# Kernel tuning notes

Measured on AMD Instinct MI355X. Metric: run time of the kernel, lower is better.

Reference implementation:

```python
import jax, jax.numpy as jnp
import numpy as np

N_VOXELS = 262144  # active output voxels (stride=1 -> same coord set as input)


def setup_inputs() -> dict:
    key = jax.random.key(0)
    k1, k2, k3, k4 = jax.random.split(key, 4)
    N, C_IN, C_OUT, K, M = N_VOXELS, 64, 64, 27, 65536
    x = jax.random.normal(k1, (N, C_IN), dtype=jnp.float32)
    W = jax.random.normal(k2, (K, C_IN, C_OUT), dtype=jnp.float32) * (1.0 / np.sqrt(C_IN * K))
    in_map = jax.random.randint(k3, (K, M), 0, N, dtype=jnp.int32)
    out_map = jax.random.randint(k4, (K, M), 0, N, dtype=jnp.int32)
    return {"x": x, "W": W, "in_map": in_map, "out_map": out_map}


def reference(x, W, in_map, out_map):
    # Sparse (Minkowski-style) convolution: gather -> per-offset GEMM -> scatter-add.
    # x: [N, Cin], W: [K, Cin, Cout], in_map/out_map: [K, M] indices into voxel list.
    N = x.shape[0]
    C_out = W.shape[-1]
    gathered = x[in_map]                              # [K, M, Cin]  (irregular gather)
    msg = jnp.einsum('kmc,kcd->kmd', gathered, W)     # [K, M, Cout] per-offset GEMM
    out = jnp.zeros((N, C_out), dtype=x.dtype)
    out = out.at[out_map.reshape(-1)].add(msg.reshape(-1, C_out))  # scatter-add
    return out
```

## Files before the change

kernel.cpp:

```cpp
#include <hip/hip_runtime.h>


typedef __attribute__((ext_vector_type(8))) short bf16x8;
typedef __attribute__((ext_vector_type(8))) unsigned short u16x8;
typedef __attribute__((ext_vector_type(4))) unsigned short u16x4;
typedef __attribute__((ext_vector_type(4))) float f32x4;
typedef __attribute__((ext_vector_type(2))) float f32x2;

constexpr int KOFF = 27;
constexpr int M = 65536;
constexpr int CIN = 64;
constexpr int COUT = 64;
constexpr int NVOX = 262144;
constexpr int NMSG = KOFF * M;
constexpr int TM_BLOCK = 512;
constexpr int TILES_PER_K = M / TM_BLOCK;
constexpr int SUBTILES = TM_BLOCK / (4 * 16);
constexpr int XCVT_BLOCKS = NVOX * CIN / 8 / 256;

static __device__ __forceinline__ short f2bf(float f) {
  unsigned u = __builtin_bit_cast(unsigned, f);
  unsigned r = (u + 0x7FFFu + ((u >> 16) & 1u)) >> 16;
  return (short)r;
}
static __device__ __forceinline__ float bf2f(unsigned short h) {
  return __builtin_bit_cast(float, (unsigned)h << 16);
}

__global__ __launch_bounds__(256) void xw_kernel(
    const float* __restrict__ x, const float* __restrict__ W,
    unsigned short* __restrict__ xb, unsigned short* __restrict__ Wf,
    int xcvtBlocks) {
  const int b = blockIdx.x;
  if (b < xcvtBlocks) {
    int i = b * 256 + threadIdx.x;
    const float4* p = (const float4*)x + (size_t)i * 2;
    float4 a = p[0], q = p[1];
    u16x8 h;
    h[0] = (unsigned short)f2bf(a.x); h[1] = (unsigned short)f2bf(a.y);
    h[2] = (unsigned short)f2bf(a.z); h[3] = (unsigned short)f2bf(a.w);
    h[4] = (unsigned short)f2bf(q.x); h[5] = (unsigned short)f2bf(q.y);
    h[6] = (unsigned short)f2bf(q.z); h[7] = (unsigned short)f2bf(q.w);
    *(u16x8*)(xb + (size_t)i * 8) = h;
  } else {
    int k = b - xcvtBlocks;
    const float* Wk = W + (size_t)k * (CIN * COUT);
    unsigned short* dst = Wf + (size_t)k * 4096;
#pragma unroll
    for (int i = 0; i < 16; ++i) {
      int e = threadIdx.x * 16 + i;
      int j = e & 7, l = (e >> 3) & 63, tu = e >> 9;
      int t = tu >> 1, u = tu & 1;
      dst[e] = (unsigned short)f2bf(Wk[(u * 32 + (l >> 4) * 8 + j) * COUT + t * 16 + (l & 15)]);
    }
  }
}

__global__ __launch_bounds__(256) void rank_kernel(const int* __restrict__ out_map,
                                                   int* __restrict__ cnt,
                                                   int* __restrict__ rank) {
  int i = (blockIdx.x * 256 + threadIdx.x) * 4;
  int4 om = *(const int4*)(out_map + i);
  int4 rk;
  rk.x = atomicAdd(&cnt[om.x], 1);
  rk.y = atomicAdd(&cnt[om.y], 1);
  rk.z = atomicAdd(&cnt[om.z], 1);
  rk.w = atomicAdd(&cnt[om.w], 1);
  *(int4*)(rank + i) = rk;
}

__global__ __launch_bounds__(256) void scan1_kernel(const int* __restrict__ cnt,
                                                    int* __restrict__ starts,
                                                    int* __restrict__ blockSums) {
  __shared__ int s[256];
  int t = threadIdx.x, i = blockIdx.x * 256 + t;
  int c = cnt[i];
  s[t] = c; __syncthreads();
  for (int off = 1; off < 256; off <<= 1) {
    int add = (t >= off) ? s[t - off] : 0;
    __syncthreads(); s[t] += add; __syncthreads();
  }
  starts[i] = s[t] - c;
  if (t == 255) blockSums[blockIdx.x] = s[t];
}

__global__ __launch_bounds__(256) void scan2_kernel(int* __restrict__ bs) {
  __shared__ int s[256];
  int t = threadIdx.x;
  int v0 = bs[t*4], v1 = bs[t*4+1], v2 = bs[t*4+2], v3 = bs[t*4+3];
  int sum = v0 + v1 + v2 + v3;
  s[t] = sum; __syncthreads();
  for (int off = 1; off < 256; off <<= 1) {
    int add = (t >= off) ? s[t - off] : 0;
    __syncthreads(); s[t] += add; __syncthreads();
  }
  int run = s[t] - sum;
  bs[t*4] = run; run += v0;
  bs[t*4+1] = run; run += v1;
  bs[t*4+2] = run; run += v2;
  bs[t*4+3] = run;
}

__global__ __launch_bounds__(256) void scan3_kernel(int* __restrict__ starts,
                                                    const int* __restrict__ blockBase) {
  int i = blockIdx.x * 256 + threadIdx.x;
  starts[i] += blockBase[blockIdx.x];
  if (i == 0) starts[NVOX] = NMSG;
}

template <bool BF16IN>
__global__ __launch_bounds__(256) void gemm_msg_kernel(
    const void* __restrict__ xin, const unsigned short* __restrict__ Wf,
    const int* __restrict__ in_map, const int* __restrict__ out_map,
    const int* __restrict__ rank, const int* __restrict__ starts,
    unsigned short* __restrict__ msg) {
  const int k = blockIdx.x / TILES_PER_K;
  const int mblock = (blockIdx.x % TILES_PER_K) * TM_BLOCK;
  const int wave = threadIdx.x >> 6;
  const int l = threadIdx.x & 63;
  const int lg = l >> 4;
  const int lr = l & 15;

  bf16x8 bfrag[4][2];
  const bf16x8* wf = (const bf16x8*)(Wf + (size_t)k * 4096);
#pragma unroll
  for (int t = 0; t < 4; ++t)
#pragma unroll
    for (int u = 0; u < 2; ++u)
      bfrag[t][u] = wf[(t * 2 + u) * 64 + l];

  const int mwave = mblock + wave * (TM_BLOCK / 4);
  const int rb = k * M + mwave;

  auto loadA = [&](int s, bf16x8& A0, bf16x8& A1) {
    int id = in_map[rb + s * 16 + lr];
    if (BF16IN) {
      const unsigned short* xr = (const unsigned short*)xin + (size_t)id * CIN + lg * 8;
      A0 = *(const bf16x8*)(xr);
      A1 = *(const bf16x8*)(xr + 32);
    } else {
      const float* xr = (const float*)xin + (size_t)id * CIN + lg * 8;
      float4 x0 = *(const float4*)(xr);
      float4 x1 = *(const float4*)(xr + 4);
      float4 x2 = *(const float4*)(xr + 32);
      float4 x3 = *(const float4*)(xr + 36);
      A0[0]=f2bf(x0.x); A0[1]=f2bf(x0.y); A0[2]=f2bf(x0.z); A0[3]=f2bf(x0.w);
      A0[4]=f2bf(x1.x); A0[5]=f2bf(x1.y); A0[6]=f2bf(x1.z); A0[7]=f2bf(x1.w);
      A1[0]=f2bf(x2.x); A1[1]=f2bf(x2.y); A1[2]=f2bf(x2.z); A1[3]=f2bf(x2.w);
      A1[4]=f2bf(x3.x); A1[5]=f2bf(x3.y); A1[6]=f2bf(x3.z); A1[7]=f2bf(x3.w);
    }
  };

  int om[4], rk[4];
#pragma unroll
  for (int r = 0; r < 4; ++r) {
    om[r] = out_map[rb + lg * 4 + r];
    rk[r] = rank[rb + lg * 4 + r];
  }

  bf16x8 c0, c1, n0, n1;
  loadA(0, c0, c1);
  loadA(1, n0, n1);

#pragma unroll 1
  for (int s = 0; s < SUBTILES; ++s) {
    bf16x8 p0, p1;
    const bool have = (s + 2 < SUBTILES);
    if (have) loadA(s + 2, p0, p1);

    int omN[4], rkN[4];
    if (s + 1 < SUBTILES) {
      const int rowb = rb + (s + 1) * 16 + lg * 4;
#pragma unroll
      for (int r = 0; r < 4; ++r) { omN[r] = out_map[rowb + r]; rkN[r] = rank[rowb + r]; }
    } else {
#pragma unroll
      for (int r = 0; r < 4; ++r) { omN[r] = 0; rkN[r] = 0; }
    }
    int st[4];
#pragma unroll
    for (int r = 0; r < 4; ++r) st[r] = starts[om[r]];

    f32x4 acc[4] = {{0.f,0.f,0.f,0.f},{0.f,0.f,0.f,0.f},{0.f,0.f,0.f,0.f},{0.f,0.f,0.f,0.f}};
#pragma unroll
    for (int t = 0; t < 4; ++t) {
      acc[t] = __builtin_amdgcn_mfma_f32_16x16x32_bf16(c0, bfrag[t][0], acc[t], 0, 0, 0);
      acc[t] = __builtin_amdgcn_mfma_f32_16x16x32_bf16(c1, bfrag[t][1], acc[t], 0, 0, 0);
    }

#pragma unroll
    for (int r = 0; r < 4; ++r) {
      const int sl = st[r] + rk[r];
      u16x4 h;
      h[0] = (unsigned short)f2bf(acc[0][r]);
      h[1] = (unsigned short)f2bf(acc[1][r]);
      h[2] = (unsigned short)f2bf(acc[2][r]);
      h[3] = (unsigned short)f2bf(acc[3][r]);
      __builtin_nontemporal_store(h, (u16x4*)(msg + (size_t)sl * 64 + lr * 4));
    }

    c0 = n0; c1 = n1;
    if (have) { n0 = p0; n1 = p1; }
#pragma unroll
    for (int r = 0; r < 4; ++r) { om[r] = omN[r]; rk[r] = rkN[r]; }
  }
}

__global__ __launch_bounds__(256) void gather_out_kernel(
    const unsigned short* __restrict__ msg, const int* __restrict__ starts,
    float* __restrict__ out) {
  const int wid = (blockIdx.x * 256 + threadIdx.x) >> 6;
  const int p = threadIdx.x & 63;
  const int r = p >> 3;
  const int c = p & 7;
  const int o = wid * 8 + r;

  const int base = starts[o];
  const int n = starts[o + 1] - base;
  const unsigned short* src = msg + (size_t)base * 64 + c * 8;

  u16x8 v[8];
#pragma unroll
  for (int i = 0; i < 8; ++i) {
    int safe = (i < n) ? i : 0;
    v[i] = __builtin_nontemporal_load((const u16x8*)(src + (size_t)safe * 64));
  }
  float acc[8] = {};
#pragma unroll
  for (int i = 0; i < 8; ++i) {
    float m = (i < n) ? 1.0f : 0.0f;
#pragma unroll
    for (int d = 0; d < 8; ++d)
      acc[d] = fmaf(m, bf2f((unsigned short)v[i][d]), acc[d]);
  }
  for (int i = 8; i < n; ++i) {
    u16x8 t = __builtin_nontemporal_load((const u16x8*)(src + (size_t)i * 64));
#pragma unroll
    for (int d = 0; d < 8; ++d) acc[d] += bf2f((unsigned short)t[d]);
  }

  float* orow = out + (size_t)o * 64 + 2 * c;
  f32x2 s0 = {acc[0], acc[4]};
  f32x2 s1 = {acc[1], acc[5]};
  f32x2 s2 = {acc[2], acc[6]};
  f32x2 s3 = {acc[3], acc[7]};
  __builtin_nontemporal_store(s0, (f32x2*)(orow));
  __builtin_nontemporal_store(s1, (f32x2*)(orow + 16));
  __builtin_nontemporal_store(s2, (f32x2*)(orow + 32));
  __builtin_nontemporal_store(s3, (f32x2*)(orow + 48));
}

__global__ __launch_bounds__(256) void spconv_atomic_kernel(
    const float* __restrict__ x, const float* __restrict__ W,
    const int* __restrict__ in_map, const int* __restrict__ out_map,
    float* __restrict__ out) {
  const int k = blockIdx.x / TILES_PER_K;
  const int mblock = (blockIdx.x % TILES_PER_K) * TM_BLOCK;
  const int wave = threadIdx.x >> 6;
  const int l = threadIdx.x & 63;
  const int lg = l >> 4;
  const int lr = l & 15;
  bf16x8 bfrag[4][2];
  const float* Wk = W + (size_t)k * (CIN * COUT);
#pragma unroll
  for (int t = 0; t < 4; ++t)
#pragma unroll
    for (int u = 0; u < 2; ++u)
#pragma unroll
      for (int j = 0; j < 8; ++j)
        bfrag[t][u][j] = f2bf(Wk[(u * 32 + lg * 8 + j) * COUT + t * 16 + lr]);
  const int mwave = mblock + wave * (TM_BLOCK / 4);
#pragma unroll 1
  for (int s = 0; s < SUBTILES; ++s) {
    const int mbase = mwave + s * 16;
    const int in_idx = in_map[k * M + mbase + lr];
    const float* xr = x + (size_t)in_idx * CIN + lg * 8;
    float4 x0 = *(const float4*)(xr);
    float4 x1 = *(const float4*)(xr + 4);
    float4 x2 = *(const float4*)(xr + 32);
    float4 x3 = *(const float4*)(xr + 36);
    bf16x8 a0, a1;
    a0[0]=f2bf(x0.x); a0[1]=f2bf(x0.y); a0[2]=f2bf(x0.z); a0[3]=f2bf(x0.w);
    a0[4]=f2bf(x1.x); a0[5]=f2bf(x1.y); a0[6]=f2bf(x1.z); a0[7]=f2bf(x1.w);
    a1[0]=f2bf(x2.x); a1[1]=f2bf(x2.y); a1[2]=f2bf(x2.z); a1[3]=f2bf(x2.w);
    a1[4]=f2bf(x3.x); a1[5]=f2bf(x3.y); a1[6]=f2bf(x3.z); a1[7]=f2bf(x3.w);
    f32x4 acc[4] = {{0.f,0.f,0.f,0.f},{0.f,0.f,0.f,0.f},{0.f,0.f,0.f,0.f},{0.f,0.f,0.f,0.f}};
#pragma unroll
    for (int t = 0; t < 4; ++t) {
      acc[t] = __builtin_amdgcn_mfma_f32_16x16x32_bf16(a0, bfrag[t][0], acc[t], 0, 0, 0);
      acc[t] = __builtin_amdgcn_mfma_f32_16x16x32_bf16(a1, bfrag[t][1], acc[t], 0, 0, 0);
    }
    const int obase = k * M + mbase + lg * 4;
    int oidx[4];
#pragma unroll
    for (int r = 0; r < 4; ++r) oidx[r] = out_map[obase + r];
#pragma unroll
    for (int t = 0; t < 4; ++t)
#pragma unroll
      for (int r = 0; r < 4; ++r)
        atomicAdd(out + (size_t)oidx[r] * COUT + t * 16 + lr, acc[t][r]);
  }
}

extern "C" void kernel_launch(void* const* d_in, const int* in_sizes, int n_in,
                              void* d_out, int out_size, void* d_ws, size_t ws_size,
                              hipStream_t stream) {
  const float* x = (const float*)d_in[0];
  const float* W = (const float*)d_in[1];
  const int* in_map = (const int*)d_in[2];
  const int* out_map = (const int*)d_in[3];
  float* out = (float*)d_out;
  char* ws = (char*)d_ws;

  const size_t msg_b    = (size_t)NMSG * 128;
  const size_t xb_b     = (size_t)NVOX * CIN * 2;
  const size_t rank_b   = (size_t)NMSG * 4;
  const size_t wf_b     = (size_t)KOFF * 4096 * 2;
  const size_t starts_b = (size_t)(NVOX + 1) * 4;
  const size_t cnt_b    = (size_t)NVOX * 4;
  auto pad = [](size_t b) { return (b + 255) & ~(size_t)255; };

  size_t need_p1 = pad(msg_b) + pad(rank_b) + pad(wf_b) + pad(starts_b);
  size_t need_p0 = need_p1 + pad(xb_b);
  bool useXb = (ws_size >= need_p0);
  bool outScratchOk = ((size_t)out_size * 4 >= cnt_b + 1024 * 4 + 256);

  if (ws_size < need_p1 || !outScratchOk) {
    hipMemsetAsync(d_out, 0, (size_t)out_size * sizeof(float), stream);
    spconv_atomic_kernel<<<dim3(KOFF * TILES_PER_K), dim3(256), 0, stream>>>(
        x, W, in_map, out_map, out);
    return;
  }

  size_t off = 0;
  unsigned short* msg = (unsigned short*)(ws + off); off += pad(msg_b);
  unsigned short* xb = nullptr;
  if (useXb) { xb = (unsigned short*)(ws + off); off += pad(xb_b); }
  int* rank = (int*)(ws + off); off += pad(rank_b);
  unsigned short* Wf = (unsigned short*)(ws + off); off += pad(wf_b);
  int* starts = (int*)(ws + off); off += pad(starts_b);

  int* cnt  = (int*)d_out;
  int* bsum = (int*)d_out + NVOX;

  hipMemsetAsync(cnt, 0, cnt_b, stream);

  int xcvtBlocks = useXb ? XCVT_BLOCKS : 0;
  xw_kernel<<<dim3(xcvtBlocks + KOFF), dim3(256), 0, stream>>>(x, W, xb, Wf, xcvtBlocks);

  rank_kernel<<<dim3(NMSG / 1024), dim3(256), 0, stream>>>(out_map, cnt, rank);

  scan1_kernel<<<dim3(NVOX / 256), dim3(256), 0, stream>>>(cnt, starts, bsum);
  scan2_kernel<<<dim3(1), dim3(256), 0, stream>>>(bsum);
  scan3_kernel<<<dim3(NVOX / 256), dim3(256), 0, stream>>>(starts, bsum);

  if (useXb)
    gemm_msg_kernel<true><<<dim3(KOFF * TILES_PER_K), dim3(256), 0, stream>>>(
        (const void*)xb, Wf, in_map, out_map, rank, starts, msg);
  else
    gemm_msg_kernel<false><<<dim3(KOFF * TILES_PER_K), dim3(256), 0, stream>>>(
        (const void*)x, Wf, in_map, out_map, rank, starts, msg);

  gather_out_kernel<<<dim3(NVOX / 32), dim3(256), 0, stream>>>(msg, starts, out);
}
```

Baseline: 228.1 us.

## Write GEMM messages in map order and gather through a sorted index list

The GEMM kernel now stores messages contiguously in original map order instead of scattering them to sorted slots. A new listscat kernel builds a permutation list (sorted slot to message index), and the gather kernel reads messages indirectly through it. The aim is to make the large msg write coalesced and to drop the out_map/rank/starts lookups from the GEMM. The cost is an extra kernel pass and random 16-byte reads in the gather, and rank moves into the output buffer as scratch.

```diff
diff --git a/kernel.cpp b/kernel.cpp
--- a/kernel.cpp
+++ b/kernel.cpp
@@ -26,6 +26,7 @@
 static __device__ __forceinline__ float bf2f(unsigned short h) {
   return __builtin_bit_cast(float, (unsigned)h << 16);
 }
+
 
 __global__ __launch_bounds__(256) void xw_kernel(
     const float* __restrict__ x, const float* __restrict__ W,
@@ -56,6 +57,7 @@
   }
 }
 
+
 __global__ __launch_bounds__(256) void rank_kernel(const int* __restrict__ out_map,
                                                    int* __restrict__ cnt,
                                                    int* __restrict__ rank) {
@@ -69,6 +71,7 @@
   *(int4*)(rank + i) = rk;
 }
 
+
 __global__ __launch_bounds__(256) void scan1_kernel(const int* __restrict__ cnt,
                                                     int* __restrict__ starts,
                                                     int* __restrict__ blockSums) {
@@ -108,12 +111,24 @@
   if (i == 0) starts[NVOX] = NMSG;
 }
 
+
+__global__ __launch_bounds__(256) void listscat_kernel(
+    const int* __restrict__ out_map, const int* __restrict__ rank,
+    const int* __restrict__ starts, int* __restrict__ list) {
+  int i = (blockIdx.x * 256 + threadIdx.x) * 4;
+  int4 om = *(const int4*)(out_map + i);
+  int4 rk = *(const int4*)(rank + i);
+  list[starts[om.x] + rk.x] = i;
+  list[starts[om.y] + rk.y] = i + 1;
+  list[starts[om.z] + rk.z] = i + 2;
+  list[starts[om.w] + rk.w] = i + 3;
+}
+
+
 template <bool BF16IN>
 __global__ __launch_bounds__(256) void gemm_msg_kernel(
     const void* __restrict__ xin, const unsigned short* __restrict__ Wf,
-    const int* __restrict__ in_map, const int* __restrict__ out_map,
-    const int* __restrict__ rank, const int* __restrict__ starts,
-    unsigned short* __restrict__ msg) {
+    const int* __restrict__ in_map, unsigned short* __restrict__ msg) {
   const int k = blockIdx.x / TILES_PER_K;
   const int mblock = (blockIdx.x % TILES_PER_K) * TM_BLOCK;
   const int wave = threadIdx.x >> 6;
@@ -151,13 +166,6 @@
     }
   };
 
-  int om[4], rk[4];
-#pragma unroll
-  for (int r = 0; r < 4; ++r) {
-    om[r] = out_map[rb + lg * 4 + r];
-    rk[r] = rank[rb + lg * 4 + r];
-  }
-
   bf16x8 c0, c1, n0, n1;
   loadA(0, c0, c1);
   loadA(1, n0, n1);
@@ -168,19 +176,6 @@
     const bool have = (s + 2 < SUBTILES);
     if (have) loadA(s + 2, p0, p1);
 
-    int omN[4], rkN[4];
-    if (s + 1 < SUBTILES) {
-      const int rowb = rb + (s + 1) * 16 + lg * 4;
-#pragma unroll
-      for (int r = 0; r < 4; ++r) { omN[r] = out_map[rowb + r]; rkN[r] = rank[rowb + r]; }
-    } else {
-#pragma unroll
-      for (int r = 0; r < 4; ++r) { omN[r] = 0; rkN[r] = 0; }
-    }
-    int st[4];
-#pragma unroll
-    for (int r = 0; r < 4; ++r) st[r] = starts[om[r]];
-
     f32x4 acc[4] = {{0.f,0.f,0.f,0.f},{0.f,0.f,0.f,0.f},{0.f,0.f,0.f,0.f},{0.f,0.f,0.f,0.f}};
 #pragma unroll
     for (int t = 0; t < 4; ++t) {
@@ -188,27 +183,26 @@
       acc[t] = __builtin_amdgcn_mfma_f32_16x16x32_bf16(c1, bfrag[t][1], acc[t], 0, 0, 0);
     }
 
+    const size_t rowb = (size_t)(rb + s * 16 + lg * 4);
 #pragma unroll
     for (int r = 0; r < 4; ++r) {
-      const int sl = st[r] + rk[r];
       u16x4 h;
       h[0] = (unsigned short)f2bf(acc[0][r]);
       h[1] = (unsigned short)f2bf(acc[1][r]);
       h[2] = (unsigned short)f2bf(acc[2][r]);
       h[3] = (unsigned short)f2bf(acc[3][r]);
-      __builtin_nontemporal_store(h, (u16x4*)(msg + (size_t)sl * 64 + lr * 4));
+      __builtin_nontemporal_store(h, (u16x4*)(msg + (rowb + r) * 64 + lr * 4));
     }
 
     c0 = n0; c1 = n1;
     if (have) { n0 = p0; n1 = p1; }
-#pragma unroll
-    for (int r = 0; r < 4; ++r) { om[r] = omN[r]; rk[r] = rkN[r]; }
-  }
-}
+  }
+}
+
 
 __global__ __launch_bounds__(256) void gather_out_kernel(
     const unsigned short* __restrict__ msg, const int* __restrict__ starts,
-    float* __restrict__ out) {
+    const int* __restrict__ list, float* __restrict__ out) {
   const int wid = (blockIdx.x * 256 + threadIdx.x) >> 6;
   const int p = threadIdx.x & 63;
   const int r = p >> 3;
@@ -217,14 +211,18 @@
 
   const int base = starts[o];
   const int n = starts[o + 1] - base;
-  const unsigned short* src = msg + (size_t)base * 64 + c * 8;
-
+
+  int li[8];
+#pragma unroll
+  for (int i = 0; i < 8; ++i) {
+    int idx = base + ((i < n) ? i : 0);
+    li[i] = list[idx < NMSG ? idx : 0];
+  }
   u16x8 v[8];
 #pragma unroll
-  for (int i = 0; i < 8; ++i) {
-    int safe = (i < n) ? i : 0;
-    v[i] = __builtin_nontemporal_load((const u16x8*)(src + (size_t)safe * 64));
-  }
+  for (int i = 0; i < 8; ++i)
+    v[i] = __builtin_nontemporal_load((const u16x8*)(msg + (size_t)li[i] * 64 + c * 8));
+
   float acc[8] = {};
 #pragma unroll
   for (int i = 0; i < 8; ++i) {
@@ -234,7 +232,8 @@
       acc[d] = fmaf(m, bf2f((unsigned short)v[i][d]), acc[d]);
   }
   for (int i = 8; i < n; ++i) {
-    u16x8 t = __builtin_nontemporal_load((const u16x8*)(src + (size_t)i * 64));
+    int idx = list[base + i];
+    u16x8 t = __builtin_nontemporal_load((const u16x8*)(msg + (size_t)idx * 64 + c * 8));
 #pragma unroll
     for (int d = 0; d < 8; ++d) acc[d] += bf2f((unsigned short)t[d]);
   }
@@ -249,6 +248,7 @@
   __builtin_nontemporal_store(s2, (f32x2*)(orow + 32));
   __builtin_nontemporal_store(s3, (f32x2*)(orow + 48));
 }
+
 
 __global__ __launch_bounds__(256) void spconv_atomic_kernel(
     const float* __restrict__ x, const float* __restrict__ W,
@@ -314,16 +314,18 @@
 
   const size_t msg_b    = (size_t)NMSG * 128;
   const size_t xb_b     = (size_t)NVOX * CIN * 2;
-  const size_t rank_b   = (size_t)NMSG * 4;
+  const size_t list_b   = (size_t)NMSG * 4;
   const size_t wf_b     = (size_t)KOFF * 4096 * 2;
   const size_t starts_b = (size_t)(NVOX + 1) * 4;
   const size_t cnt_b    = (size_t)NVOX * 4;
+  const size_t rank_b   = (size_t)NMSG * 4;
   auto pad = [](size_t b) { return (b + 255) & ~(size_t)255; };
 
-  size_t need_p1 = pad(msg_b) + pad(rank_b) + pad(wf_b) + pad(starts_b);
+  size_t need_p1 = pad(msg_b) + pad(list_b) + pad(wf_b) + pad(starts_b);
   size_t need_p0 = need_p1 + pad(xb_b);
   bool useXb = (ws_size >= need_p0);
-  bool outScratchOk = ((size_t)out_size * 4 >= cnt_b + 1024 * 4 + 256);
+  bool outScratchOk =
+      ((size_t)out_size * 4 >= pad(cnt_b) + pad(1024 * 4) + pad(rank_b));
 
   if (ws_size < need_p1 || !outScratchOk) {
     hipMemsetAsync(d_out, 0, (size_t)out_size * sizeof(float), stream);
@@ -336,12 +338,15 @@
   unsigned short* msg = (unsigned short*)(ws + off); off += pad(msg_b);
   unsigned short* xb = nullptr;
   if (useXb) { xb = (unsigned short*)(ws + off); off += pad(xb_b); }
-  int* rank = (int*)(ws + off); off += pad(rank_b);
+  int* list = (int*)(ws + off); off += pad(list_b);
   unsigned short* Wf = (unsigned short*)(ws + off); off += pad(wf_b);
   int* starts = (int*)(ws + off); off += pad(starts_b);
 
-  int* cnt  = (int*)d_out;
-  int* bsum = (int*)d_out + NVOX;
+  char* outs = (char*)d_out;
+  size_t ooff = 0;
+  int* cnt  = (int*)(outs + ooff); ooff += pad(cnt_b);
+  int* bsum = (int*)(outs + ooff); ooff += pad(1024 * 4);
+  int* rank = (int*)(outs + ooff);
 
   hipMemsetAsync(cnt, 0, cnt_b, stream);
 
@@ -354,12 +359,14 @@
   scan2_kernel<<<dim3(1), dim3(256), 0, stream>>>(bsum);
   scan3_kernel<<<dim3(NVOX / 256), dim3(256), 0, stream>>>(starts, bsum);
 
+  listscat_kernel<<<dim3(NMSG / 1024), dim3(256), 0, stream>>>(out_map, rank, starts, list);
+
   if (useXb)
     gemm_msg_kernel<true><<<dim3(KOFF * TILES_PER_K), dim3(256), 0, stream>>>(
-        (const void*)xb, Wf, in_map, out_map, rank, starts, msg);
+        (const void*)xb, Wf, in_map, msg);
   else
     gemm_msg_kernel<false><<<dim3(KOFF * TILES_PER_K), dim3(256), 0, stream>>>(
-        (const void*)x, Wf, in_map, out_map, rank, starts, msg);
-
-  gather_out_kernel<<<dim3(NVOX / 32), dim3(256), 0, stream>>>(msg, starts, out);
-}
+        (const void*)x, Wf, in_map, msg);
+
+  gather_out_kernel<<<dim3(NVOX / 32), dim3(256), 0, stream>>>(msg, starts, list, out);
+}
```

Measured after the change: 259.9 us. +14.0%, slower.
